# Kernel optimization log

Measured on AMD Instinct MI355X. Metric: run time of the kernel, lower is better.

## Reference

```python
import jax, jax.numpy as jnp
import numpy as np

B = 2048      # number of ragged rows
R = 10        # row size: 1 anchor + 1 pos + 8 negatives
D = 1024      # embedding dim
ALPHA = 1.0
BETA = 0.5
TEMP = 0.05


def setup_inputs() -> dict:
    key = jax.random.key(0)
    k1, k2 = jax.random.split(key)
    embeddings = jax.random.normal(k1, (B * R, D), dtype=jnp.float32)
    scores = jax.random.normal(k2, (B * (R - 1),), dtype=jnp.float32)
    row_sizes = jnp.full((B,), R, dtype=jnp.int64)
    return {"embeddings": embeddings, "scores": scores, "row_sizes": row_sizes}


def _l2norm(x, eps=1e-12):
    return x / jnp.maximum(jnp.linalg.norm(x, axis=-1, keepdims=True), eps)


def reference(embeddings, scores, row_sizes):
    b = row_sizes.shape[0]
    r = embeddings.shape[0] // b           # uniform row size
    d = embeddings.shape[1]
    emb = embeddings.reshape(b, r, d)
    anchor = emb[:, 0]                      # [B, D]
    pos = emb[:, 1]                         # [B, D]
    negs = emb[:, 2:]                       # [B, R-2, D]

    # per-row cosine similarities: anchor vs pos, anchor vs each neg
    a_n = _l2norm(anchor)
    pos_score = jnp.sum(a_n * _l2norm(pos), axis=-1)                 # [B]
    neg_scores = jnp.einsum('bd,bkd->bk', a_n, _l2norm(negs))        # [B, R-2]
    row_scores = jnp.concatenate([pos_score[:, None], neg_scores], axis=1)  # [B, R-1]

    # KLDivLoss(reduction='batchmean') per row: sum(t*(log t - log p)) / (R-1)
    log_p = jax.nn.log_softmax(row_scores, axis=1)
    ce = jax.nn.softmax(scores.reshape(b, r - 1), axis=1)
    kl_per_row = jnp.sum(jax.scipy.special.xlogy(ce, ce) - ce * log_p, axis=1) / (r - 1)
    loss = BETA * jnp.mean(kl_per_row)

    # single InfoNCE over the whole batch: targets = [pos; all negs]
    targets = jnp.concatenate([pos, negs.reshape(b * (r - 2), d)], axis=0)  # [B*(R-1), D]
    sim = (a_n @ _l2norm(targets).T) / TEMP                                 # [B, B*(R-1)]
    logz = jax.nn.logsumexp(sim, axis=1)
    diag = sim[jnp.arange(b), jnp.arange(b)]
    ce_loss = jnp.mean(logz - diag)
    loss = loss + ALPHA * ce_loss
    return loss
```

## Files before the change

kernel.cpp:

```cpp
#include <hip/hip_runtime.h>
#include <hip/hip_bf16.h>
#include <stdint.h>

#define NB 2048
#define NR 10
#define ND 1024
#define NTGT (NB * (NR - 1))
#define INV_TEMP 20.0f

#define BM 128
#define BN 256
#define BK 64
#define NKT (ND / BK)
#define TM_TILES (NB / BM)
#define TN_TILES (NTGT / BN)

typedef __attribute__((ext_vector_type(4))) float floatx4;
typedef __attribute__((ext_vector_type(2))) long longx2;

#define BAR()    asm volatile("s_barrier" ::: "memory")
#define LGKM0()  asm volatile("s_waitcnt lgkmcnt(0)" ::: "memory")
#define VMCNT0() asm volatile("s_waitcnt vmcnt(0)" ::: "memory")

__device__ __forceinline__ void async16(const void* g, void* l) {
  __builtin_amdgcn_global_load_lds(
      (const __attribute__((address_space(1))) unsigned int*)g,
      (__attribute__((address_space(3))) unsigned int*)l,
      16, 0, 0);
}

__global__ __launch_bounds__(256) void prep_kernel(
    const float* __restrict__ emb, const float* __restrict__ scores,
    unsigned char* __restrict__ A8, unsigned char* __restrict__ T8,
    float* __restrict__ pos_score, float* __restrict__ kl_out) {
  int b = blockIdx.x;
  int tid = threadIdx.x;
  int wid = tid >> 6, lane = tid & 63;
  const float* base = emb + (size_t)b * NR * ND;

  float4 v[NR];
  float ss[NR], dt[NR - 1];
#pragma unroll
  for (int r = 0; r < NR; ++r) {
    v[r] = reinterpret_cast<const float4*>(base + (size_t)r * ND)[tid];
    ss[r] = v[r].x * v[r].x + v[r].y * v[r].y + v[r].z * v[r].z + v[r].w * v[r].w;
  }
#pragma unroll
  for (int t = 0; t < NR - 1; ++t)
    dt[t] = v[0].x * v[t + 1].x + v[0].y * v[t + 1].y + v[0].z * v[t + 1].z +
            v[0].w * v[t + 1].w;

#pragma unroll
  for (int off = 32; off; off >>= 1) {
#pragma unroll
    for (int r = 0; r < NR; ++r) ss[r] += __shfl_xor(ss[r], off, 64);
#pragma unroll
    for (int t = 0; t < NR - 1; ++t) dt[t] += __shfl_xor(dt[t], off, 64);
  }
  __shared__ float red[4][2 * NR - 1];
  if (lane == 0) {
#pragma unroll
    for (int r = 0; r < NR; ++r) red[wid][r] = ss[r];
#pragma unroll
    for (int t = 0; t < NR - 1; ++t) red[wid][NR + t] = dt[t];
  }
  __syncthreads();

  float inv[NR];
#pragma unroll
  for (int r = 0; r < NR; ++r) {
    float s = red[0][r] + red[1][r] + red[2][r] + red[3][r];
    inv[r] = 1.0f / fmaxf(sqrtf(s), 1e-12f);
  }

#pragma unroll
  for (int r = 0; r < NR; ++r) {
    unsigned char* dst;
    if (r == 0)      dst = A8 + (size_t)b * ND;
    else if (r == 1) dst = T8 + (size_t)b * ND;
    else             dst = T8 + (size_t)(NB + b * 8 + (r - 2)) * ND;
    int p = 0;
    p = __builtin_amdgcn_cvt_pk_fp8_f32(v[r].x * inv[r], v[r].y * inv[r], p, false);
    p = __builtin_amdgcn_cvt_pk_fp8_f32(v[r].z * inv[r], v[r].w * inv[r], p, true);
    reinterpret_cast<int*>(dst)[tid] = p;
  }

  if (tid == 0) {
    float rs[NR - 1];
#pragma unroll
    for (int t = 0; t < NR - 1; ++t) {
      float d = red[0][NR + t] + red[1][NR + t] + red[2][NR + t] + red[3][NR + t];
      rs[t] = d * inv[0] * inv[t + 1];
    }
    float sc[NR - 1], ms = -1e30f;
#pragma unroll
    for (int k = 0; k < NR - 1; ++k) { sc[k] = scores[b * (NR - 1) + k]; ms = fmaxf(ms, sc[k]); }
    float se = 0.f;
#pragma unroll
    for (int k = 0; k < NR - 1; ++k) { sc[k] = expf(sc[k] - ms); se += sc[k]; }
    float mr = -1e30f;
#pragma unroll
    for (int k = 0; k < NR - 1; ++k) mr = fmaxf(mr, rs[k]);
    float sr = 0.f;
#pragma unroll
    for (int k = 0; k < NR - 1; ++k) sr += expf(rs[k] - mr);
    float lz = logf(sr) + mr;
    float kl = 0.f;
#pragma unroll
    for (int k = 0; k < NR - 1; ++k) {
      float ce = sc[k] / se;
      kl += ce * logf(ce) - ce * (rs[k] - lz);
    }
    kl_out[b] = kl / (float)(NR - 1);
    pos_score[b] = rs[0];
  }
}


__device__ __forceinline__ void stage_A8(const unsigned char* __restrict__ gtile,
                                         unsigned char* lds, int k0, int tid) {
  int lrow = tid >> 2;
  int u = (tid & 3) ^ ((lrow >> 1) & 3);
  const unsigned char* src = gtile + (size_t)lrow * ND + k0 + u * 16;
  unsigned char* dst = lds + (tid & ~63) * 16;
  async16(src, dst);
}

__device__ __forceinline__ void stage_B8(const unsigned char* __restrict__ gtile,
                                         unsigned char* lds, int k0, int tid) {
#pragma unroll
  for (int r = 0; r < 2; ++r) {
    int slot = r * 512 + tid;
    int lrow = slot >> 2;
    int u = (slot & 3) ^ ((lrow >> 1) & 3);
    const unsigned char* src = gtile + (size_t)lrow * ND + k0 + u * 16;
    unsigned char* dst = lds + (r * 512 + (tid & ~63)) * 16;
    async16(src, dst);
  }
}

__device__ __forceinline__ longx2 frag8(const unsigned char* lds, int row, int lq) {
  int byte = row * 64 + ((lq * 16) ^ (((row >> 1) & 3) << 4));
  return *reinterpret_cast<const longx2*>(lds + byte);
}

__global__ __launch_bounds__(512, 4) void gemm_lse_kernel(
    const unsigned char* __restrict__ A, const unsigned char* __restrict__ T,
    float* __restrict__ sumexp) {
  __shared__ unsigned char smem[2 * (BM + BN) * BK];

  int bid = blockIdx.x;
  int xcd = bid & 7;
  int j = bid >> 3;
  int tn = xcd * 9 + (j >> 4);
  int tm = j & 15;

  int tid = threadIdx.x;
  int wid = tid >> 6, lane = tid & 63;
  int wm = wid >> 2, wn = wid & 3;
  int lrow = lane & 15, lq = lane >> 4;

  const unsigned char* Ag = A + (size_t)tm * BM * ND;
  const unsigned char* Tg = T + (size_t)tn * BN * ND;

  floatx4 acc[4][4] = {};

  unsigned char* As0 = smem;
  unsigned char* Bs0 = smem + BM * BK;
  unsigned char* As1 = smem + (BM + BN) * BK;
  unsigned char* Bs1 = smem + (2 * BM + BN) * BK;

  stage_A8(Ag, As0, 0, tid);
  stage_B8(Tg, Bs0, 0, tid);
  VMCNT0();
  BAR();

#pragma unroll 2
  for (int s = 0; s < NKT; ++s) {
    const int buf = s & 1;
    const unsigned char* Asb = buf ? As1 : As0;
    const unsigned char* Bsb = buf ? Bs1 : Bs0;
    unsigned char* Asn = buf ? As0 : As1;
    unsigned char* Bsn = buf ? Bs0 : Bs1;
    const int kn = ((s + 1) & (NKT - 1)) * BK;

    longx2 aF[4], bF[2];

    stage_A8(Ag, Asn, kn, tid);
    stage_B8(Tg, Bsn, kn, tid);
#pragma unroll
    for (int m = 0; m < 4; ++m)
      aF[m] = frag8(Asb, wm * 64 + m * 16 + lrow, lq);
#pragma unroll
    for (int n = 0; n < 2; ++n)
      bF[n] = frag8(Bsb, wn * 64 + n * 16 + lrow, lq);
    BAR();
    LGKM0();
    __builtin_amdgcn_s_setprio(1);
#pragma unroll
    for (int m = 0; m < 4; ++m)
#pragma unroll
      for (int n = 0; n < 2; ++n) {
        acc[m][n] = __builtin_amdgcn_mfma_f32_16x16x32_fp8_fp8(aF[m].x, bF[n].x, acc[m][n], 0, 0, 0);
        acc[m][n] = __builtin_amdgcn_mfma_f32_16x16x32_fp8_fp8(aF[m].y, bF[n].y, acc[m][n], 0, 0, 0);
      }
    __builtin_amdgcn_s_setprio(0);
    BAR();

#pragma unroll
    for (int n = 0; n < 2; ++n)
      bF[n] = frag8(Bsb, wn * 64 + (n + 2) * 16 + lrow, lq);
    BAR();
    LGKM0();
    __builtin_amdgcn_s_setprio(1);
#pragma unroll
    for (int m = 0; m < 4; ++m)
#pragma unroll
      for (int n = 0; n < 2; ++n) {
        acc[m][n + 2] = __builtin_amdgcn_mfma_f32_16x16x32_fp8_fp8(aF[m].x, bF[n].x, acc[m][n + 2], 0, 0, 0);
        acc[m][n + 2] = __builtin_amdgcn_mfma_f32_16x16x32_fp8_fp8(aF[m].y, bF[n].y, acc[m][n + 2], 0, 0, 0);
      }
    __builtin_amdgcn_s_setprio(0);
    __builtin_amdgcn_sched_barrier(0);
    VMCNT0();
    BAR();
  }

  VMCNT0();

#pragma unroll
  for (int m = 0; m < 4; ++m) {
#pragma unroll
    for (int j2 = 0; j2 < 4; ++j2) {
      float s = __expf(acc[m][0][j2] * INV_TEMP) + __expf(acc[m][1][j2] * INV_TEMP) +
                __expf(acc[m][2][j2] * INV_TEMP) + __expf(acc[m][3][j2] * INV_TEMP);
      s += __shfl_xor(s, 1, 64);
      s += __shfl_xor(s, 2, 64);
      s += __shfl_xor(s, 4, 64);
      s += __shfl_xor(s, 8, 64);
      if (lrow == 0) {
        int grow = tm * BM + wm * 64 + m * 16 + lq * 4 + j2;
        atomicAdd(&sumexp[grow], s);
      }
    }
  }
}

__global__ __launch_bounds__(256) void finalize_kernel(
    const float* __restrict__ sumexp, const float* __restrict__ pos_score,
    const float* __restrict__ kl, float* __restrict__ out) {
  int tid = threadIdx.x;
  float kls = 0.f, ces = 0.f;
  for (int i = tid; i < NB; i += 256) {
    kls += kl[i];
    ces += logf(sumexp[i]) - pos_score[i] * INV_TEMP;
  }
#pragma unroll
  for (int off = 32; off; off >>= 1) {
    kls += __shfl_xor(kls, off, 64);
    ces += __shfl_xor(ces, off, 64);
  }
  __shared__ float sk[4], se4[4];
  int wid = tid >> 6, lane = tid & 63;
  if (lane == 0) { sk[wid] = kls; se4[wid] = ces; }
  __syncthreads();
  if (tid == 0) {
    float k4 = sk[0] + sk[1] + sk[2] + sk[3];
    float e4 = se4[0] + se4[1] + se4[2] + se4[3];
    out[0] = 0.5f * (k4 / (float)NB) + 1.0f * (e4 / (float)NB);
  }
}

extern "C" void kernel_launch(void* const* d_in, const int* in_sizes, int n_in,
                              void* d_out, int out_size, void* d_ws, size_t ws_size,
                              hipStream_t stream) {
  const float* emb = (const float*)d_in[0];
  const float* scores = (const float*)d_in[1];
  float* out = (float*)d_out;

  char* ws = (char*)d_ws;
  size_t offA = 0;
  size_t offT = offA + (size_t)NB * ND;
  size_t offSum = offT + (size_t)NTGT * ND;
  size_t offPos = offSum + (size_t)NB * 4;
  size_t offKl = offPos + (size_t)NB * 4;

  unsigned char* A8 = (unsigned char*)(ws + offA);
  unsigned char* T8 = (unsigned char*)(ws + offT);
  float* sumexp = (float*)(ws + offSum);
  float* pos_score = (float*)(ws + offPos);
  float* kl = (float*)(ws + offKl);

  hipMemsetAsync(sumexp, 0, (size_t)NB * 4, stream);
  prep_kernel<<<NB, 256, 0, stream>>>(emb, scores, A8, T8, pos_score, kl);
  gemm_lse_kernel<<<dim3(TM_TILES * TN_TILES), 512, 0, stream>>>(A8, T8, sumexp);
  finalize_kernel<<<1, 256, 0, stream>>>(sumexp, pos_score, kl, out);
}
```

Measured before the change: 97.94 us.

## Triple-buffer LDS staging in the FP8 GEMM with a partial vmcnt wait

The GEMM main loop moves from double to triple buffering of the A/B LDS tiles, prefetching two K-steps ahead. It waits with vmcnt(3), so only the older stage's three async loads per thread must finish. The loop now reads all four B fragments at once, which removes the split half-tile MFMA phases and two of the three barriers per iteration. In exchange, LDS per block grows by half, which may cut how many blocks fit on a CU, and more fragment registers are live at once.

After: 90.85 us. 7.2% less time.

```diff
diff --git a/kernel.cpp b/kernel.cpp
--- a/kernel.cpp
+++ b/kernel.cpp
@@ -19,8 +19,8 @@
 typedef __attribute__((ext_vector_type(2))) long longx2;
 
 #define BAR()    asm volatile("s_barrier" ::: "memory")
-#define LGKM0()  asm volatile("s_waitcnt lgkmcnt(0)" ::: "memory")
 #define VMCNT0() asm volatile("s_waitcnt vmcnt(0)" ::: "memory")
+#define VMCNT3() asm volatile("s_waitcnt vmcnt(3)" ::: "memory")
 
 __device__ __forceinline__ void async16(const void* g, void* l) {
   __builtin_amdgcn_global_load_lds(
@@ -147,7 +147,7 @@
 __global__ __launch_bounds__(512, 4) void gemm_lse_kernel(
     const unsigned char* __restrict__ A, const unsigned char* __restrict__ T,
     float* __restrict__ sumexp) {
-  __shared__ unsigned char smem[2 * (BM + BN) * BK];
+  __shared__ unsigned char smem[3 * (BM + BN) * BK];
 
   int bid = blockIdx.x;
   int xcd = bid & 7;
@@ -165,65 +165,54 @@
 
   floatx4 acc[4][4] = {};
 
-  unsigned char* As0 = smem;
-  unsigned char* Bs0 = smem + BM * BK;
-  unsigned char* As1 = smem + (BM + BN) * BK;
-  unsigned char* Bs1 = smem + (2 * BM + BN) * BK;
-
-  stage_A8(Ag, As0, 0, tid);
-  stage_B8(Tg, Bs0, 0, tid);
-  VMCNT0();
+  unsigned char* bufA0 = smem;
+  unsigned char* bufB0 = smem + BM * BK;
+  unsigned char* bufA1 = smem + (BM + BN) * BK;
+  unsigned char* bufB1 = bufA1 + BM * BK;
+  unsigned char* bufA2 = smem + 2 * (BM + BN) * BK;
+  unsigned char* bufB2 = bufA2 + BM * BK;
+
+  stage_A8(Ag, bufA0, 0, tid);
+  stage_B8(Tg, bufB0, 0, tid);
+  stage_A8(Ag, bufA1, BK, tid);
+  stage_B8(Tg, bufB1, BK, tid);
+  VMCNT3();
   BAR();
 
-#pragma unroll 2
+  const unsigned char* Acur = bufA0;  const unsigned char* Bcur = bufB0;
+  unsigned char* Anxt = bufA1;        unsigned char* Bnxt = bufB1;
+  unsigned char* Afar = bufA2;        unsigned char* Bfar = bufB2;
+
   for (int s = 0; s < NKT; ++s) {
-    const int buf = s & 1;
-    const unsigned char* Asb = buf ? As1 : As0;
-    const unsigned char* Bsb = buf ? Bs1 : Bs0;
-    unsigned char* Asn = buf ? As0 : As1;
-    unsigned char* Bsn = buf ? Bs0 : Bs1;
-    const int kn = ((s + 1) & (NKT - 1)) * BK;
-
-    longx2 aF[4], bF[2];
-
-    stage_A8(Ag, Asn, kn, tid);
-    stage_B8(Tg, Bsn, kn, tid);
+    const int kn = ((s + 2) & (NKT - 1)) * BK;
+    stage_A8(Ag, Afar, kn, tid);
+    stage_B8(Tg, Bfar, kn, tid);
+
+    longx2 aF[4], bF[4];
 #pragma unroll
     for (int m = 0; m < 4; ++m)
-      aF[m] = frag8(Asb, wm * 64 + m * 16 + lrow, lq);
-#pragma unroll
-    for (int n = 0; n < 2; ++n)
-      bF[n] = frag8(Bsb, wn * 64 + n * 16 + lrow, lq);
-    BAR();
-    LGKM0();
+      aF[m] = frag8(Acur, wm * 64 + m * 16 + lrow, lq);
+#pragma unroll
+    for (int n = 0; n < 4; ++n)
+      bF[n] = frag8(Bcur, wn * 64 + n * 16 + lrow, lq);
+
     __builtin_amdgcn_s_setprio(1);
 #pragma unroll
     for (int m = 0; m < 4; ++m)
 #pragma unroll
-      for (int n = 0; n < 2; ++n) {
+      for (int n = 0; n < 4; ++n) {
         acc[m][n] = __builtin_amdgcn_mfma_f32_16x16x32_fp8_fp8(aF[m].x, bF[n].x, acc[m][n], 0, 0, 0);
         acc[m][n] = __builtin_amdgcn_mfma_f32_16x16x32_fp8_fp8(aF[m].y, bF[n].y, acc[m][n], 0, 0, 0);
       }
     __builtin_amdgcn_s_setprio(0);
+
+    VMCNT3();
     BAR();
 
-#pragma unroll
-    for (int n = 0; n < 2; ++n)
-      bF[n] = frag8(Bsb, wn * 64 + (n + 2) * 16 + lrow, lq);
-    BAR();
-    LGKM0();
-    __builtin_amdgcn_s_setprio(1);
-#pragma unroll
-    for (int m = 0; m < 4; ++m)
-#pragma unroll
-      for (int n = 0; n < 2; ++n) {
-        acc[m][n + 2] = __builtin_amdgcn_mfma_f32_16x16x32_fp8_fp8(aF[m].x, bF[n].x, acc[m][n + 2], 0, 0, 0);
-        acc[m][n + 2] = __builtin_amdgcn_mfma_f32_16x16x32_fp8_fp8(aF[m].y, bF[n].y, acc[m][n + 2], 0, 0, 0);
-      }
-    __builtin_amdgcn_s_setprio(0);
-    __builtin_amdgcn_sched_barrier(0);
-    VMCNT0();
-    BAR();
+    unsigned char* ta = (unsigned char*)Acur;  unsigned char* tb = (unsigned char*)Bcur;
+    Acur = Anxt;  Bcur = Bnxt;
+    Anxt = Afar;  Bnxt = Bfar;
+    Afar = ta;    Bfar = tb;
   }
 
   VMCNT0();
```
